# Kernel optimization log

Hardware: AMD Instinct MI355X
Metric: run time of the kernel (lower is better)

## Reference

```python
import jax, jax.numpy as jnp
import numpy as np

N, E, D_IN, D_H, L = 50000, 600000, 256, 128, 3


def setup_inputs() -> dict:
    key = jax.random.key(0)
    ks = jax.random.split(key, 10)
    w = lambda k, *sh: jax.random.normal(k, sh, jnp.float32) * 0.05
    z = lambda *sh: jnp.zeros(sh, jnp.float32)
    return {
        "x": jax.random.normal(ks[0], (N, D_IN), jnp.float32),
        "edge_index": jax.random.randint(ks[1], (2, E), 0, N),
        # input projection
        "w_in": w(ks[2], D_IN, D_H), "b_in": z(D_H),
        # stacked GCNConv weights/biases for L layers
        "w_gcn": w(ks[3], L, D_H, D_H), "b_gcn": z(L, D_H),
        # node classifier MLP
        "w_nc1": w(ks[4], D_H, D_H), "b_nc1": z(D_H),
        "w_nc2": w(ks[5], D_H, 1), "b_nc2": z(1),
        # origin classifier MLP
        "w_oc1": w(ks[6], D_H, D_H), "b_oc1": z(D_H),
        "w_oc2": w(ks[7], D_H, 1), "b_oc2": z(1),
    }


def _forward(x, edge_index, w_in, b_in, w_gcn, b_gcn,
             w_nc1, b_nc1, w_nc2, b_nc2, w_oc1, b_oc1, w_oc2, b_oc2):
    # GCNConv default: add self loops, symmetric D^{-1/2} (A+I) D^{-1/2} normalization
    loops = jnp.arange(N)
    row = jnp.concatenate([edge_index[0], loops])  # source nodes
    col = jnp.concatenate([edge_index[1], loops])  # target nodes
    deg = jax.ops.segment_sum(jnp.ones_like(col, x.dtype), col, num_segments=N)
    dinv = jnp.where(deg > 0, jax.lax.rsqrt(deg), 0.0)
    norm = dinv[row] * dinv[col]                   # [E+N]

    h = jax.nn.relu(x @ w_in + b_in)               # [N, D_H]
    for l in range(L):
        xw = h @ w_gcn[l]                          # linear transform first (PyG order)
        agg = jax.ops.segment_sum(xw[row] * norm[:, None], col, num_segments=N)
        h = jax.nn.relu(h + agg + b_gcn[l])        # residual + relu; dropout=identity (eval)

    def mlp_sig(h, w1, b1, w2, b2):
        return jax.nn.sigmoid(jax.nn.relu(h @ w1 + b1) @ w2 + b2)[:, 0]

    node_pred = mlp_sig(h, w_nc1, b_nc1, w_nc2, b_nc2)
    origin_pred = mlp_sig(h, w_oc1, b_oc1, w_oc2, b_oc2)
    error_type_pred = jnp.zeros((N, 4), x.dtype)
    return node_pred, origin_pred, error_type_pred, h


def reference(x, edge_index, w_in, b_in, w_gcn, b_gcn,
              w_nc1, b_nc1, w_nc2, b_nc2, w_oc1, b_oc1, w_oc2, b_oc2):
    return _forward(x, edge_index, w_in, b_in, w_gcn, b_gcn,
                    w_nc1, b_nc1, w_nc2, b_nc2, w_oc1, b_oc1, w_oc2, b_oc2)
```

## Files before the change

### kernel.cpp

```cpp
#include <hip/hip_runtime.h>
#include <math.h>

#define DH 128
#define ELLCAP 48

typedef short short8 __attribute__((ext_vector_type(8)));
typedef float f32x4 __attribute__((ext_vector_type(4)));

__device__ __forceinline__ unsigned short f2bu(float f) {
  unsigned int u = __builtin_bit_cast(unsigned int, f);
  unsigned int r = (u + 0x7fffu + ((u >> 16) & 1u)) >> 16;
  return (unsigned short)r;
}
__device__ __forceinline__ float blo(unsigned int u) {
  return __builtin_bit_cast(float, u << 16);
}
__device__ __forceinline__ float bhi(unsigned int u) {
  return __builtin_bit_cast(float, u & 0xffff0000u);
}
__device__ __forceinline__ unsigned int packb2(float a, float b) {
  return (unsigned int)f2bu(a) | ((unsigned int)f2bu(b) << 16);
}


__global__ __launch_bounds__(256) void prep_kernel(
    const float* __restrict__ w_in, const float* __restrict__ w_gcn,
    const float* __restrict__ w_nc1, const float* __restrict__ w_oc1,
    const float* __restrict__ x,
    unsigned short* __restrict__ w_inT, unsigned short* __restrict__ w_gcnT,
    unsigned short* __restrict__ w_nc1T, unsigned short* __restrict__ w_oc1T,
    unsigned short* __restrict__ xb,
    int* __restrict__ cnt, float* __restrict__ out_err, int n) {
  int idx = blockIdx.x * 256 + threadIdx.x;
  if (idx < 32768) {
    int k = idx >> 7, c = idx & 127;
    w_inT[c * 256 + k] = f2bu(w_in[idx]);
  } else if (idx < 81920) {
    int sub = idx - 32768;
    int off = sub & 16383;
    int k = off >> 7, c = off & 127;
    w_gcnT[(sub >> 14) * 16384 + c * 128 + k] = f2bu(w_gcn[sub]);
  } else if (idx < 98304) {
    int off = idx - 81920;
    int k = off >> 7, c = off & 127;
    w_nc1T[c * 128 + k] = f2bu(w_nc1[off]);
  } else if (idx < 114688) {
    int off = idx - 98304;
    int k = off >> 7, c = off & 127;
    w_oc1T[c * 128 + k] = f2bu(w_oc1[off]);
  } else if (idx < 114688 + n) {
    cnt[idx - 114688] = 0;
  } else if (idx < 114688 + 5 * n) {
    out_err[idx - 114688 - n] = 0.f;
  } else {
    int c = idx - (114688 + 5 * n);
    if (c < n * 64) {
      float4 v = *(const float4*)&x[(size_t)c * 4];
      unsigned short o[4] = {f2bu(v.x), f2bu(v.y), f2bu(v.z), f2bu(v.w)};
      *(uint2*)&xb[(size_t)c * 4] = *(const uint2*)o;
    }
  }
}


template <int K, int MODE>
__device__ __forceinline__ void gemm_tile(const unsigned short* __restrict__ A,
                                          const unsigned short* __restrict__ WT,
                                          const float* __restrict__ bias,
                                          const int* __restrict__ cnt,
                                          unsigned short* __restrict__ Cb, int n,
                                          int bid, int t) {
  const int lane = t & 63;
  const int w = t >> 6;
  const int wr = w >> 1, wc = w & 1;
  const int lr = lane & 15, lg = lane >> 4;
  const int r_base = bid * 128 + wr * 64;
  const int c_base = wc * 64;

  f32x4 acc[4][4] = {};

#pragma unroll
  for (int kk = 0; kk < K / 32; kk++) {
    const int koff = kk * 32 + lg * 8;
    short8 a[4], b[4];
#pragma unroll
    for (int m = 0; m < 4; m++) {
      int row = r_base + m * 16 + lr;
      row = row < n ? row : n - 1;
      a[m] = *(const short8*)&A[(size_t)row * K + koff];
    }
#pragma unroll
    for (int nb = 0; nb < 4; nb++) {
      int col = c_base + nb * 16 + lr;
      b[nb] = *(const short8*)&WT[(size_t)col * K + koff];
    }
#pragma unroll
    for (int m = 0; m < 4; m++)
#pragma unroll
      for (int nb = 0; nb < 4; nb++)
        acc[m][nb] = __builtin_amdgcn_mfma_f32_16x16x32_bf16(a[m], b[nb], acc[m][nb], 0, 0, 0);
  }

  float bcol[4];
  if (MODE != 0) {
#pragma unroll
    for (int nb = 0; nb < 4; nb++) bcol[nb] = bias[c_base + nb * 16 + lr];
  }

#pragma unroll
  for (int m = 0; m < 4; m++) {
#pragma unroll
    for (int i = 0; i < 4; i++) {
      int row = r_base + m * 16 + lg * 4 + i;
      if (row < n) {
        float sc = 0.f;
        if (MODE == 0) sc = rsqrtf((float)(cnt[row] + 1));
#pragma unroll
        for (int nb = 0; nb < 4; nb++) {
          int col = c_base + nb * 16 + lr;
          float v = acc[m][nb][i];
          if (MODE == 0) {
            Cb[(size_t)row * DH + col] = f2bu(v * sc);
          } else {
            v = fmaxf(v + bcol[nb], 0.f);
            Cb[(size_t)row * DH + col] = f2bu(v);
          }
        }
      }
    }
  }
}


__global__ __launch_bounds__(256) void count_ingemm_kernel(
    const int* __restrict__ erow, const int* __restrict__ ecol,
    int* __restrict__ cnt, unsigned short* __restrict__ ell, int e,
    const unsigned short* __restrict__ xb, const unsigned short* __restrict__ w_inT,
    const float* __restrict__ b_in, unsigned short* __restrict__ hb, int n, int CB) {
  if ((int)blockIdx.x < CB) {
    const int stride = CB * 256;
    int i = blockIdx.x * 256 + threadIdx.x;
    for (; i + 3 * stride < e; i += 4 * stride) {
      int c0 = ecol[i], c1 = ecol[i + stride];
      int c2 = ecol[i + 2 * stride], c3 = ecol[i + 3 * stride];
      int r0 = erow[i], r1 = erow[i + stride];
      int r2 = erow[i + 2 * stride], r3 = erow[i + 3 * stride];
      int p0 = atomicAdd(&cnt[c0], 1);
      int p1 = atomicAdd(&cnt[c1], 1);
      int p2 = atomicAdd(&cnt[c2], 1);
      int p3 = atomicAdd(&cnt[c3], 1);
      if (p0 < ELLCAP) ell[(size_t)c0 * ELLCAP + p0] = (unsigned short)r0;
      if (p1 < ELLCAP) ell[(size_t)c1 * ELLCAP + p1] = (unsigned short)r1;
      if (p2 < ELLCAP) ell[(size_t)c2 * ELLCAP + p2] = (unsigned short)r2;
      if (p3 < ELLCAP) ell[(size_t)c3 * ELLCAP + p3] = (unsigned short)r3;
    }
    for (; i < e; i += stride) {
      int c = ecol[i];
      int pos = atomicAdd(&cnt[c], 1);
      if (pos < ELLCAP) ell[(size_t)c * ELLCAP + pos] = (unsigned short)erow[i];
    }
  } else {
    gemm_tile<256, 1>(xb, w_inT, b_in, nullptr, hb, n, blockIdx.x - CB, threadIdx.x);
  }
}


template <int K, int MODE>
__global__ __launch_bounds__(256) void gemm_kernel(const unsigned short* __restrict__ A,
                                                   const unsigned short* __restrict__ WT,
                                                   const float* __restrict__ bias,
                                                   const int* __restrict__ cnt,
                                                   unsigned short* __restrict__ Cb, int n) {
  gemm_tile<K, MODE>(A, WT, bias, cnt, Cb, n, blockIdx.x, threadIdx.x);
}


__global__ __launch_bounds__(256) void agg_kernel(const uint2* __restrict__ xwb2,
                                                  const int* __restrict__ cnt,
                                                  const unsigned short* __restrict__ ell,
                                                  const float* __restrict__ bias,
                                                  uint2* __restrict__ hb2,
                                                  float* __restrict__ hout, int n) {
  const int node = blockIdx.x * 4 + (threadIdx.x >> 6);
  if (node >= n) return;
  const int lane = threadIdx.x & 63;
  const int half = lane >> 5;
  const int cidx = lane & 31;
  const int degc = cnt[node];
  const float self = rsqrtf((float)(degc + 1));
  const int deg = degc < ELLCAP ? degc : ELLCAP;
  const unsigned short* el = ell + (size_t)node * ELLCAP;

  uint2 hu = make_uint2(0u, 0u);
  if (half == 0) hu = hb2[(size_t)node * 32 + cidx];

  float a0, a1, a2, a3;
  if (half == 0) {
    uint2 su = xwb2[(size_t)node * 32 + cidx];
    a0 = blo(su.x); a1 = bhi(su.x);
    a2 = blo(su.y); a3 = bhi(su.y);
  } else {
    a0 = a1 = a2 = a3 = 0.f;
  }

  int j = 0;
  for (; j + 16 <= deg; j += 16) {
    int s[8];
#pragma unroll
    for (int k = 0; k < 8; k++) s[k] = el[j + 2 * k + half];
    uint2 u[8];
#pragma unroll
    for (int k = 0; k < 8; k++) u[k] = xwb2[(size_t)s[k] * 32 + cidx];
#pragma unroll
    for (int k = 0; k < 8; k++) {
      a0 += blo(u[k].x); a1 += bhi(u[k].x);
      a2 += blo(u[k].y); a3 += bhi(u[k].y);
    }
  }
  for (; j + 8 <= deg; j += 8) {
    int s0 = el[j + half], s1 = el[j + 2 + half];
    int s2 = el[j + 4 + half], s3 = el[j + 6 + half];
    uint2 u0 = xwb2[(size_t)s0 * 32 + cidx];
    uint2 u1 = xwb2[(size_t)s1 * 32 + cidx];
    uint2 u2 = xwb2[(size_t)s2 * 32 + cidx];
    uint2 u3 = xwb2[(size_t)s3 * 32 + cidx];
    a0 += blo(u0.x); a1 += bhi(u0.x); a2 += blo(u0.y); a3 += bhi(u0.y);
    a0 += blo(u1.x); a1 += bhi(u1.x); a2 += blo(u1.y); a3 += bhi(u1.y);
    a0 += blo(u2.x); a1 += bhi(u2.x); a2 += blo(u2.y); a3 += bhi(u2.y);
    a0 += blo(u3.x); a1 += bhi(u3.x); a2 += blo(u3.y); a3 += bhi(u3.y);
  }
  for (; j < deg; j += 2) {
    int jj = j + half;
    if (jj < deg) {
      int s = el[jj];
      uint2 u = xwb2[(size_t)s * 32 + cidx];
      a0 += blo(u.x); a1 += bhi(u.x); a2 += blo(u.y); a3 += bhi(u.y);
    }
  }

  a0 += __shfl_xor(a0, 32);
  a1 += __shfl_xor(a1, 32);
  a2 += __shfl_xor(a2, 32);
  a3 += __shfl_xor(a3, 32);

  if (half == 0) {
    const float4 bv = *(const float4*)&bias[cidx * 4];
    float r0 = fmaxf(blo(hu.x) + self * a0 + bv.x, 0.f);
    float r1 = fmaxf(bhi(hu.x) + self * a1 + bv.y, 0.f);
    float r2 = fmaxf(blo(hu.y) + self * a2 + bv.z, 0.f);
    float r3 = fmaxf(bhi(hu.y) + self * a3 + bv.w, 0.f);
    hb2[(size_t)node * 32 + cidx] = make_uint2(packb2(r0, r1), packb2(r2, r3));
    if (hout) *(float4*)&hout[(size_t)node * DH + cidx * 4] = make_float4(r0, r1, r2, r3);
  }
}


__global__ __launch_bounds__(256) void heads_kernel(
    const unsigned short* __restrict__ hb,
    const unsigned short* __restrict__ w1T_a, const float* __restrict__ b1_a,
    const float* __restrict__ w2_a, const float* __restrict__ b2_a,
    const unsigned short* __restrict__ w1T_b, const float* __restrict__ b1_b,
    const float* __restrict__ w2_b, const float* __restrict__ b2_b,
    float* __restrict__ out_a, float* __restrict__ out_b, int n) {
  const int t = threadIdx.x;
  const int lane = t & 63;
  const int w = t >> 6;
  const int lr = lane & 15, lg = lane >> 4;
  const int r_base = blockIdx.x * 128 + w * 32;

#pragma unroll
  for (int head = 0; head < 2; head++) {
    const unsigned short* W1T = head ? w1T_b : w1T_a;
    const float* b1 = head ? b1_b : b1_a;
    const float* w2 = head ? w2_b : w2_a;
    const float b2 = head ? b2_b[0] : b2_a[0];
    float* out = head ? out_b : out_a;

    f32x4 acc[2][8] = {};
#pragma unroll
    for (int kk = 0; kk < 4; kk++) {
      const int koff = kk * 32 + lg * 8;
      short8 a[2];
#pragma unroll
      for (int m = 0; m < 2; m++) {
        int row = r_base + m * 16 + lr;
        row = row < n ? row : n - 1;
        a[m] = *(const short8*)&hb[(size_t)row * DH + koff];
      }
#pragma unroll
      for (int nb = 0; nb < 8; nb++) {
        short8 b = *(const short8*)&W1T[(size_t)(nb * 16 + lr) * DH + koff];
#pragma unroll
        for (int m = 0; m < 2; m++)
          acc[m][nb] = __builtin_amdgcn_mfma_f32_16x16x32_bf16(a[m], b, acc[m][nb], 0, 0, 0);
      }
    }

    float b1v[8], w2v[8];
#pragma unroll
    for (int nb = 0; nb < 8; nb++) {
      b1v[nb] = b1[nb * 16 + lr];
      w2v[nb] = w2[nb * 16 + lr];
    }

#pragma unroll
    for (int m = 0; m < 2; m++) {
#pragma unroll
      for (int i = 0; i < 4; i++) {
        float s = 0.f;
#pragma unroll
        for (int nb = 0; nb < 8; nb++)
          s += fmaxf(acc[m][nb][i] + b1v[nb], 0.f) * w2v[nb];
        s += __shfl_xor(s, 1);
        s += __shfl_xor(s, 2);
        s += __shfl_xor(s, 4);
        s += __shfl_xor(s, 8);
        int row = r_base + m * 16 + lg * 4 + i;
        if (lr == 0 && row < n) out[row] = 1.f / (1.f + __expf(-(s + b2)));
      }
    }
  }
}


extern "C" void kernel_launch(void* const* d_in, const int* in_sizes, int n_in,
                              void* d_out, int out_size, void* d_ws, size_t ws_size,
                              hipStream_t stream) {
  const float* x     = (const float*)d_in[0];
  const int*   ei    = (const int*)d_in[1];
  const float* w_in  = (const float*)d_in[2];
  const float* b_in  = (const float*)d_in[3];
  const float* w_gcn = (const float*)d_in[4];
  const float* b_gcn = (const float*)d_in[5];
  const float* w_nc1 = (const float*)d_in[6];
  const float* b_nc1 = (const float*)d_in[7];
  const float* w_nc2 = (const float*)d_in[8];
  const float* b_nc2 = (const float*)d_in[9];
  const float* w_oc1 = (const float*)d_in[10];
  const float* b_oc1 = (const float*)d_in[11];
  const float* w_oc2 = (const float*)d_in[12];
  const float* b_oc2 = (const float*)d_in[13];

  const int N = in_sizes[0] / 256;
  const int E = in_sizes[1] / 2;
  const int* erow = ei;
  const int* ecol = ei + E;

  float* out      = (float*)d_out;
  float* out_node = out;
  float* out_orig = out + N;
  float* out_err  = out + 2 * (size_t)N;
  float* h        = out + 6 * (size_t)N;

  unsigned short* xwb = (unsigned short*)d_ws;
  unsigned short* hb  = xwb + (size_t)N * DH;
  unsigned short* xb  = hb + (size_t)N * DH;
  unsigned short* w_inT  = xb + (size_t)N * 256;
  unsigned short* w_gcnT = w_inT + 128 * 256;
  unsigned short* w_nc1T = w_gcnT + 3 * 128 * 128;
  unsigned short* w_oc1T = w_nc1T + 128 * 128;
  int* cnt = (int*)(w_oc1T + 128 * 128);
  unsigned short* ell = (unsigned short*)(cnt + N);

  const int prepTot = 114688 + 5 * N + N * 64;
  prep_kernel<<<(prepTot + 255) / 256, 256, 0, stream>>>(
      w_in, w_gcn, w_nc1, w_oc1, x, w_inT, w_gcnT, w_nc1T, w_oc1T, xb,
      cnt, out_err, N);

  const int gb = (N + 127) / 128;
  const int CB = 192;

  count_ingemm_kernel<<<CB + gb, 256, 0, stream>>>(erow, ecol, cnt, ell, E,
                                                   xb, w_inT, b_in, hb, N, CB);

  for (int l = 0; l < 3; l++) {
    gemm_kernel<128, 0><<<gb, 256, 0, stream>>>(hb, w_gcnT + (size_t)l * DH * DH,
                                                nullptr, cnt, xwb, N);
    agg_kernel<<<(N + 3) / 4, 256, 0, stream>>>((const uint2*)xwb, cnt, ell,
                                                b_gcn + (size_t)l * DH, (uint2*)hb,
                                                l == 2 ? h : nullptr, N);
  }
  heads_kernel<<<gb, 256, 0, stream>>>(hb, w_nc1T, b_nc1, w_nc2, b_nc2,
                                       w_oc1T, b_oc1, w_oc2, b_oc2,
                                       out_node, out_orig, N);
}
```

Measured before the change: 226.6 us.

## Pad ELL lists with a zero-row sentinel to drop aggregation tail loops

Fills every ELL slot with a sentinel index N that points to an added all-zero row in the xw buffer. The aggregation kernel can then always process groups of 16 neighbors without tail handling. The edge-scatter loop is also unrolled to 8 atomics per iteration, and the number of count blocks goes from 192 to 288. The cost is an extra memset-like pass over the ELL array in prep and wasted loads of the zero row for padded slots.

```diff
diff --git a/kernel.cpp b/kernel.cpp
--- a/kernel.cpp
+++ b/kernel.cpp
@@ -30,7 +30,8 @@
     unsigned short* __restrict__ w_inT, unsigned short* __restrict__ w_gcnT,
     unsigned short* __restrict__ w_nc1T, unsigned short* __restrict__ w_oc1T,
     unsigned short* __restrict__ xb,
-    int* __restrict__ cnt, float* __restrict__ out_err, int n) {
+    int* __restrict__ cnt, float* __restrict__ out_err,
+    unsigned int* __restrict__ ell32, unsigned int* __restrict__ xwb_zrow, int n) {
   int idx = blockIdx.x * 256 + threadIdx.x;
   if (idx < 32768) {
     int k = idx >> 7, c = idx & 127;
@@ -52,13 +53,17 @@
     cnt[idx - 114688] = 0;
   } else if (idx < 114688 + 5 * n) {
     out_err[idx - 114688 - n] = 0.f;
-  } else {
+  } else if (idx < 114688 + 69 * n) {
     int c = idx - (114688 + 5 * n);
-    if (c < n * 64) {
-      float4 v = *(const float4*)&x[(size_t)c * 4];
-      unsigned short o[4] = {f2bu(v.x), f2bu(v.y), f2bu(v.z), f2bu(v.w)};
-      *(uint2*)&xb[(size_t)c * 4] = *(const uint2*)o;
-    }
+    float4 v = *(const float4*)&x[(size_t)c * 4];
+    unsigned short o[4] = {f2bu(v.x), f2bu(v.y), f2bu(v.z), f2bu(v.w)};
+    *(uint2*)&xb[(size_t)c * 4] = *(const uint2*)o;
+  } else if (idx < 114688 + 69 * n + (n * ELLCAP) / 2) {
+    int c = idx - (114688 + 69 * n);
+    unsigned int s = (unsigned int)n;
+    ell32[c] = s | (s << 16);
+  } else if (idx < 114688 + 69 * n + (n * ELLCAP) / 2 + 64) {
+    xwb_zrow[idx - (114688 + 69 * n + (n * ELLCAP) / 2)] = 0u;
   }
 }
 
@@ -140,19 +145,18 @@
   if ((int)blockIdx.x < CB) {
     const int stride = CB * 256;
     int i = blockIdx.x * 256 + threadIdx.x;
-    for (; i + 3 * stride < e; i += 4 * stride) {
-      int c0 = ecol[i], c1 = ecol[i + stride];
-      int c2 = ecol[i + 2 * stride], c3 = ecol[i + 3 * stride];
-      int r0 = erow[i], r1 = erow[i + stride];
-      int r2 = erow[i + 2 * stride], r3 = erow[i + 3 * stride];
-      int p0 = atomicAdd(&cnt[c0], 1);
-      int p1 = atomicAdd(&cnt[c1], 1);
-      int p2 = atomicAdd(&cnt[c2], 1);
-      int p3 = atomicAdd(&cnt[c3], 1);
-      if (p0 < ELLCAP) ell[(size_t)c0 * ELLCAP + p0] = (unsigned short)r0;
-      if (p1 < ELLCAP) ell[(size_t)c1 * ELLCAP + p1] = (unsigned short)r1;
-      if (p2 < ELLCAP) ell[(size_t)c2 * ELLCAP + p2] = (unsigned short)r2;
-      if (p3 < ELLCAP) ell[(size_t)c3 * ELLCAP + p3] = (unsigned short)r3;
+    for (; i + 7 * stride < e; i += 8 * stride) {
+      int c[8], r[8], p[8];
+#pragma unroll
+      for (int k = 0; k < 8; k++) {
+        c[k] = ecol[i + k * stride];
+        r[k] = erow[i + k * stride];
+      }
+#pragma unroll
+      for (int k = 0; k < 8; k++) p[k] = atomicAdd(&cnt[c[k]], 1);
+#pragma unroll
+      for (int k = 0; k < 8; k++)
+        if (p[k] < ELLCAP) ell[(size_t)c[k] * ELLCAP + p[k]] = (unsigned short)r[k];
     }
     for (; i < e; i += stride) {
       int c = ecol[i];
@@ -203,8 +207,7 @@
     a0 = a1 = a2 = a3 = 0.f;
   }
 
-  int j = 0;
-  for (; j + 16 <= deg; j += 16) {
+  for (int j = 0; j < deg; j += 16) {
     int s[8];
 #pragma unroll
     for (int k = 0; k < 8; k++) s[k] = el[j + 2 * k + half];
@@ -215,26 +218,6 @@
     for (int k = 0; k < 8; k++) {
       a0 += blo(u[k].x); a1 += bhi(u[k].x);
       a2 += blo(u[k].y); a3 += bhi(u[k].y);
-    }
-  }
-  for (; j + 8 <= deg; j += 8) {
-    int s0 = el[j + half], s1 = el[j + 2 + half];
-    int s2 = el[j + 4 + half], s3 = el[j + 6 + half];
-    uint2 u0 = xwb2[(size_t)s0 * 32 + cidx];
-    uint2 u1 = xwb2[(size_t)s1 * 32 + cidx];
-    uint2 u2 = xwb2[(size_t)s2 * 32 + cidx];
-    uint2 u3 = xwb2[(size_t)s3 * 32 + cidx];
-    a0 += blo(u0.x); a1 += bhi(u0.x); a2 += blo(u0.y); a3 += bhi(u0.y);
-    a0 += blo(u1.x); a1 += bhi(u1.x); a2 += blo(u1.y); a3 += bhi(u1.y);
-    a0 += blo(u2.x); a1 += bhi(u2.x); a2 += blo(u2.y); a3 += bhi(u2.y);
-    a0 += blo(u3.x); a1 += bhi(u3.x); a2 += blo(u3.y); a3 += bhi(u3.y);
-  }
-  for (; j < deg; j += 2) {
-    int jj = j + half;
-    if (jj < deg) {
-      int s = el[jj];
-      uint2 u = xwb2[(size_t)s * 32 + cidx];
-      a0 += blo(u.x); a1 += bhi(u.x); a2 += blo(u.y); a3 += bhi(u.y);
     }
   }
 
@@ -353,7 +336,7 @@
   float* h        = out + 6 * (size_t)N;
 
   unsigned short* xwb = (unsigned short*)d_ws;
-  unsigned short* hb  = xwb + (size_t)N * DH;
+  unsigned short* hb  = xwb + ((size_t)N + 1) * DH;
   unsigned short* xb  = hb + (size_t)N * DH;
   unsigned short* w_inT  = xb + (size_t)N * 256;
   unsigned short* w_gcnT = w_inT + 128 * 256;
@@ -362,13 +345,13 @@
   int* cnt = (int*)(w_oc1T + 128 * 128);
   unsigned short* ell = (unsigned short*)(cnt + N);
 
-  const int prepTot = 114688 + 5 * N + N * 64;
+  const int prepTot = 114688 + 69 * N + (N * ELLCAP) / 2 + 64;
   prep_kernel<<<(prepTot + 255) / 256, 256, 0, stream>>>(
       w_in, w_gcn, w_nc1, w_oc1, x, w_inT, w_gcnT, w_nc1T, w_oc1T, xb,
-      cnt, out_err, N);
+      cnt, out_err, (unsigned int*)ell, (unsigned int*)(xwb + (size_t)N * DH), N);
 
   const int gb = (N + 127) / 128;
-  const int CB = 192;
+  const int CB = 288;
 
   count_ingemm_kernel<<<CB + gb, 256, 0, stream>>>(erow, ecol, cnt, ell, E,
                                                    xb, w_inT, b_in, hb, N, CB);
```

Measured after the change: 219.7 us. -3.0%, faster.
